# Kernel optimization log

Hardware: AMD Instinct MI355X
Metric: run time of the kernel (lower is better)

Reference implementation:

```python
import jax, jax.numpy as jnp
import numpy as np


def _bilinear_grid_sample(fea, grid):
    """torch.nn.functional.grid_sample, mode=bilinear, padding_mode=zeros, align_corners=False.
    fea: (B,C,H,W); grid: (B,Hg,Wg,2) with xy in [-1,1]. Returns (B,C,Hg,Wg)."""
    B, C, H, W = fea.shape
    Hg, Wg = grid.shape[1], grid.shape[2]
    gx, gy = grid[..., 0], grid[..., 1]
    # unnormalize (align_corners=False)
    x = ((gx + 1.0) * W - 1.0) * 0.5
    y = ((gy + 1.0) * H - 1.0) * 0.5
    x0 = jnp.floor(x); y0 = jnp.floor(y)
    x1 = x0 + 1.0;     y1 = y0 + 1.0
    wx1 = x - x0; wx0 = 1.0 - wx1
    wy1 = y - y0; wy0 = 1.0 - wy1
    flat = fea.reshape(B, C, H * W)

    def corner(xi, yi, w):
        valid = (xi >= 0) & (xi <= W - 1) & (yi >= 0) & (yi <= H - 1)
        xi_c = jnp.clip(xi, 0, W - 1).astype(jnp.int32)
        yi_c = jnp.clip(yi, 0, H - 1).astype(jnp.int32)
        idx = (yi_c * W + xi_c).reshape(B, 1, Hg * Wg)
        v = jnp.take_along_axis(flat, jnp.broadcast_to(idx, (B, C, Hg * Wg)), axis=2)
        return v * (w * valid.astype(fea.dtype)).reshape(B, 1, Hg * Wg)

    out = (corner(x0, y0, wx0 * wy0) + corner(x1, y0, wx1 * wy0)
           + corner(x0, y1, wx0 * wy1) + corner(x1, y1, wx1 * wy1))
    return out.reshape(B, C, Hg, Wg)


def _conv1d_k1(x, W, b):
    # x: (B,Cin,N), W: (Cout,Cin), b: (Cout,) -> (B,Cout,N)
    return jnp.einsum('oc,bcn->bon', W, x) + b[None, :, None]


def setup_inputs() -> dict:
    key = jax.random.key(0)
    ks = jax.random.split(key, 8)
    B, C, H, W = 4, 16, 90, 160
    N_s, N_anchor, N_y = 8, 200, 20
    scale = 8
    fea = jax.random.normal(ks[0], (B, C, H, W), dtype=jnp.float32)
    sampled_3d_points = jax.random.normal(ks[1], (N_s, B, N_anchor, N_y, 4), dtype=jnp.float32)
    # 2D pixel coords at full resolution: x in [0, W*scale), y in [0, H*scale)
    u = jax.random.uniform(ks[2], (N_s, B, N_anchor, N_y, 2), dtype=jnp.float32)
    points_2d_coord = u * jnp.array([W * scale, H * scale], dtype=jnp.float32)
    W_local = jax.random.normal(ks[3], (16, 16), dtype=jnp.float32) * 0.25
    b_local = jax.random.normal(ks[4], (16,), dtype=jnp.float32) * 0.01
    W_emb = jax.random.normal(ks[5], (256, 4), dtype=jnp.float32) * 0.5
    b_emb = jax.random.normal(ks[6], (256,), dtype=jnp.float32) * 0.01
    return {"fea": fea, "sampled_3d_points": sampled_3d_points,
            "points_2d_coord": points_2d_coord,
            "W_local": W_local, "b_local": b_local,
            "W_emb": W_emb, "b_emb": b_emb, "scale": scale}


def reference(fea, sampled_3d_points, points_2d_coord, W_local, b_local, W_emb, b_emb, scale):
    B, C, H, W = fea.shape
    N_s, _, N_anchor, N_y, _ = points_2d_coord.shape
    # normalize 2D coords to [-1,1] grid
    norm_weight = jnp.array([1.0 / W, 1.0 / H], dtype=fea.dtype)
    ner = (points_2d_coord / scale) * norm_weight * 2.0 - 1.0
    ner = jnp.transpose(ner, (1, 0, 2, 3, 4)).reshape(B, N_s * N_anchor, N_y, 2)
    local_fea = _bilinear_grid_sample(fea, ner)            # (B,C,N_s*N_anchor,N_y)
    local_fea = local_fea.reshape(B, C, -1)                # (B,C,N)
    local_fea = _conv1d_k1(local_fea, W_local, b_local)    # (B,16,N)
    # point embedding: permute(1,4,0,2,3) -> (B,4,N_s,N_anchor,N_y)
    sp = jnp.transpose(sampled_3d_points, (1, 4, 0, 2, 3)).reshape(B, 4, -1)
    embedded_points = _conv1d_k1(sp, W_emb, b_emb)         # (B,256,N)
    return (embedded_points, local_fea)
```

## Files before the change

### kernel.cpp

```cpp
#include <hip/hip_runtime.h>

#define B_    4
#define C_    16
#define H_    90
#define W_    160
#define NS_   8
#define NA_   200
#define NY_   20
#define NPB_  (NS_*NA_*NY_)
#define NPB4_ (NPB_/4)
#define CO_   256
#define EMB_ELEMS ((size_t)B_*CO_*NPB_)
#define SCALE_F 8.0f
#define HW_   (H_*W_)

#define EMB_BLOCKS 1000
#define LOC_BLOCKS 500
#define TOTAL_BLOCKS (EMB_BLOCKS + LOC_BLOCKS)

typedef float f32x4 __attribute__((ext_vector_type(4)));

__device__ __forceinline__ void nt_store4(const float4& v, float4* dst) {
    f32x4 r = { v.x, v.y, v.z, v.w };
    __builtin_nontemporal_store(r, (f32x4*)dst);
}

__global__ __launch_bounds__(256) void fused_local_emb_kernel(
    const float*  __restrict__ fea,
    const float4* __restrict__ sp3d,
    const float2* __restrict__ pc2d,
    const float*  __restrict__ W_local,
    const float*  __restrict__ b_local,
    const float4* __restrict__ W_emb,
    const float*  __restrict__ b_emb,
    float* __restrict__ out)
{
    __shared__ float  sPx[256], sPy[256], sPz[256], sPw[256];
    __shared__ float4 sWe[128];
    __shared__ float  sbe[128];
    __shared__ float sWl[256];
    __shared__ float sbl[16];
    __shared__ float sV[16*256];

    const int tid = threadIdx.x;
    const int idx = blockIdx.x;
    const int l  = tid & 63;
    const int wv = tid >> 6;

    const int grp = idx / 3;
    const int r3  = idx - grp*3;

    if (r3 != 2) {
        const int emb_id = grp*2 + r3;
        const int b    = emb_id / 250;
        const int rem0 = emb_id - b*250;
        const int tile = rem0 >> 1;
        const int half = rem0 & 1;

        if (tid < 128) {
            sWe[tid] = W_emb[half*128 + tid];
            sbe[tid] = b_emb[half*128 + tid];
        }

        const int n = tile*256 + tid;
        const int s = n / (NA_*NY_);
        const int r = n - s*(NA_*NY_);
        const float4 p = sp3d[s*(B_*NA_*NY_) + b*(NA_*NY_) + r];
        sPx[tid] = p.x; sPy[tid] = p.y; sPz[tid] = p.z; sPw[tid] = p.w;
        __syncthreads();

        const float4 PX = ((const float4*)sPx)[l];
        const float4 PY = ((const float4*)sPy)[l];
        const float4 PZ = ((const float4*)sPz)[l];
        const float4 PW = ((const float4*)sPw)[l];

        float4* eo4 = (float4*)(out + (size_t)b*CO_*NPB_) + tile*64;
        const int m0 = wv*32;
#pragma unroll 8
        for (int oi = 0; oi < 32; ++oi) {
            const int m = m0 + oi;
            const int o = half*128 + m;
            const float4 w = sWe[m];
            const float bb = sbe[m];
            float4 rr;
            rr.x = fmaf(w.w, PW.x, fmaf(w.z, PZ.x, fmaf(w.y, PY.x, fmaf(w.x, PX.x, bb))));
            rr.y = fmaf(w.w, PW.y, fmaf(w.z, PZ.y, fmaf(w.y, PY.y, fmaf(w.x, PX.y, bb))));
            rr.z = fmaf(w.w, PW.z, fmaf(w.z, PZ.z, fmaf(w.y, PY.z, fmaf(w.x, PX.z, bb))));
            rr.w = fmaf(w.w, PW.w, fmaf(w.z, PZ.w, fmaf(w.y, PY.w, fmaf(w.x, PX.w, bb))));
            nt_store4(rr, &eo4[(size_t)o*NPB4_ + l]);
        }
        return;
    }

    const int lid  = grp;
    const int b    = lid / 125;
    const int tile = lid - b*125;
    const int n    = tile*256 + tid;

    sWl[tid] = W_local[tid];
    if (tid < 16) sbl[tid] = b_local[tid];

    const int s   = n / (NA_*NY_);
    const int rem = n - s*(NA_*NY_);
    const int a   = rem / NY_;
    const int yy  = rem - a*NY_;

    const float2 pc = pc2d[((s*B_ + b)*NA_ + a)*NY_ + yy];

    const float gx = (pc.x / SCALE_F) * (1.0f/(float)W_) * 2.0f - 1.0f;
    const float gy = (pc.y / SCALE_F) * (1.0f/(float)H_) * 2.0f - 1.0f;
    const float xf = ((gx + 1.0f) * (float)W_ - 1.0f) * 0.5f;
    const float yf = ((gy + 1.0f) * (float)H_ - 1.0f) * 0.5f;

    const float x0f = floorf(xf), y0f = floorf(yf);
    const float x1f = x0f + 1.0f, y1f = y0f + 1.0f;
    const float wx1 = xf - x0f, wx0 = 1.0f - wx1;
    const float wy1 = yf - y0f, wy0 = 1.0f - wy1;

    const float vx0 = (x0f >= 0.0f && x0f <= (float)(W_-1)) ? 1.0f : 0.0f;
    const float vx1 = (x1f >= 0.0f && x1f <= (float)(W_-1)) ? 1.0f : 0.0f;
    const float vy0 = (y0f >= 0.0f && y0f <= (float)(H_-1)) ? 1.0f : 0.0f;
    const float vy1 = (y1f >= 0.0f && y1f <= (float)(H_-1)) ? 1.0f : 0.0f;

    const int xi0 = (int)fminf(fmaxf(x0f, 0.0f), (float)(W_-1));
    const int xi1 = (int)fminf(fmaxf(x1f, 0.0f), (float)(W_-1));
    const int yi0 = (int)fminf(fmaxf(y0f, 0.0f), (float)(H_-1));
    const int yi1 = (int)fminf(fmaxf(y1f, 0.0f), (float)(H_-1));

    const float w00 = wx0*wy0*vx0*vy0;
    const float w01 = wx1*wy0*vx1*vy0;
    const float w10 = wx0*wy1*vx0*vy1;
    const float w11 = wx1*wy1*vx1*vy1;

    const int i00 = yi0*W_ + xi0;
    const int i01 = yi0*W_ + xi1;
    const int i10 = yi1*W_ + xi0;
    const int i11 = yi1*W_ + xi1;

    const float* fb = fea + b*(C_*HW_);
    float f00[16], f01[16], f10[16], f11[16];
#pragma unroll
    for (int c = 0; c < 16; ++c) {
        const float* fc = fb + c*HW_;
        f00[c] = fc[i00];
        f01[c] = fc[i01];
        f10[c] = fc[i10];
        f11[c] = fc[i11];
    }

    float v[16];
#pragma unroll
    for (int c = 0; c < 16; ++c)
        v[c] = w00*f00[c] + w01*f01[c] + w10*f10[c] + w11*f11[c];
#pragma unroll
    for (int c = 0; c < 16; ++c)
        sV[c*256 + tid] = v[c];

    __syncthreads();

    float4 acc[4];
#pragma unroll
    for (int k = 0; k < 4; ++k) {
        const float bk = sbl[4*wv + k];
        acc[k].x = bk; acc[k].y = bk; acc[k].z = bk; acc[k].w = bk;
    }
#pragma unroll
    for (int c = 0; c < 16; ++c) {
        const float4 sv = ((const float4*)(sV + c*256))[l];
#pragma unroll
        for (int k = 0; k < 4; ++k) {
            const float wl = sWl[(4*wv + k)*16 + c];
            acc[k].x = fmaf(wl, sv.x, acc[k].x);
            acc[k].y = fmaf(wl, sv.y, acc[k].y);
            acc[k].z = fmaf(wl, sv.z, acc[k].z);
            acc[k].w = fmaf(wl, sv.w, acc[k].w);
        }
    }
    float4* lo4 = (float4*)(out + EMB_ELEMS + (size_t)b*16*NPB_ + tile*256);
#pragma unroll
    for (int k = 0; k < 4; ++k)
        nt_store4(acc[k], &lo4[(4*wv + k)*NPB4_ + l]);
}

extern "C" void kernel_launch(void* const* d_in, const int* in_sizes, int n_in,
                              void* d_out, int out_size, void* d_ws, size_t ws_size,
                              hipStream_t stream) {
    const float* fea     = (const float*)d_in[0];
    const float4* sp3d   = (const float4*)d_in[1];
    const float2* pc2d   = (const float2*)d_in[2];
    const float* W_local = (const float*)d_in[3];
    const float* b_local = (const float*)d_in[4];
    const float4* W_emb  = (const float4*)d_in[5];
    const float* b_emb   = (const float*)d_in[6];

    dim3 grid(TOTAL_BLOCKS);
    dim3 block(256);
    fused_local_emb_kernel<<<grid, block, 0, stream>>>(
        fea, sp3d, pc2d, W_local, b_local, W_emb, b_emb, (float*)d_out);
}
```

Baseline: 36.98 us.

## Merge grid-sample work into half of the embedding blocks to overlap gathers with stores

```diff
diff --git a/kernel.cpp b/kernel.cpp
--- a/kernel.cpp
+++ b/kernel.cpp
@@ -14,9 +14,7 @@
 #define SCALE_F 8.0f
 #define HW_   (H_*W_)
 
-#define EMB_BLOCKS 1000
-#define LOC_BLOCKS 500
-#define TOTAL_BLOCKS (EMB_BLOCKS + LOC_BLOCKS)
+#define TOTAL_BLOCKS 1000
 
 typedef float f32x4 __attribute__((ext_vector_type(4)));
 
@@ -38,148 +36,140 @@
     __shared__ float  sPx[256], sPy[256], sPz[256], sPw[256];
     __shared__ float4 sWe[128];
     __shared__ float  sbe[128];
-    __shared__ float sWl[256];
-    __shared__ float sbl[16];
-    __shared__ float sV[16*256];
+    __shared__ float  sWl[256];
+    __shared__ float  sbl[16];
+    __shared__ float  sV[16*256];
 
     const int tid = threadIdx.x;
-    const int idx = blockIdx.x;
+    const int blk = blockIdx.x;
+    const int b    = blk / 250;
+    const int rem0 = blk - b*250;
+    const int tile = rem0 >> 1;
+    const int half = rem0 & 1;
     const int l  = tid & 63;
     const int wv = tid >> 6;
 
-    const int grp = idx / 3;
-    const int r3  = idx - grp*3;
-
-    if (r3 != 2) {
-        const int emb_id = grp*2 + r3;
-        const int b    = emb_id / 250;
-        const int rem0 = emb_id - b*250;
-        const int tile = rem0 >> 1;
-        const int half = rem0 & 1;
-
-        if (tid < 128) {
-            sWe[tid] = W_emb[half*128 + tid];
-            sbe[tid] = b_emb[half*128 + tid];
-        }
-
-        const int n = tile*256 + tid;
-        const int s = n / (NA_*NY_);
-        const int r = n - s*(NA_*NY_);
-        const float4 p = sp3d[s*(B_*NA_*NY_) + b*(NA_*NY_) + r];
-        sPx[tid] = p.x; sPy[tid] = p.y; sPz[tid] = p.z; sPw[tid] = p.w;
-        __syncthreads();
-
-        const float4 PX = ((const float4*)sPx)[l];
-        const float4 PY = ((const float4*)sPy)[l];
-        const float4 PZ = ((const float4*)sPz)[l];
-        const float4 PW = ((const float4*)sPw)[l];
-
-        float4* eo4 = (float4*)(out + (size_t)b*CO_*NPB_) + tile*64;
-        const int m0 = wv*32;
-#pragma unroll 8
-        for (int oi = 0; oi < 32; ++oi) {
-            const int m = m0 + oi;
-            const int o = half*128 + m;
-            const float4 w = sWe[m];
-            const float bb = sbe[m];
-            float4 rr;
-            rr.x = fmaf(w.w, PW.x, fmaf(w.z, PZ.x, fmaf(w.y, PY.x, fmaf(w.x, PX.x, bb))));
-            rr.y = fmaf(w.w, PW.y, fmaf(w.z, PZ.y, fmaf(w.y, PY.y, fmaf(w.x, PX.y, bb))));
-            rr.z = fmaf(w.w, PW.z, fmaf(w.z, PZ.z, fmaf(w.y, PY.z, fmaf(w.x, PX.z, bb))));
-            rr.w = fmaf(w.w, PW.w, fmaf(w.z, PZ.w, fmaf(w.y, PY.w, fmaf(w.x, PX.w, bb))));
-            nt_store4(rr, &eo4[(size_t)o*NPB4_ + l]);
-        }
-        return;
+    if (tid < 128) {
+        sWe[tid] = W_emb[half*128 + tid];
+        sbe[tid] = b_emb[half*128 + tid];
+    }
+    if (half == 0) {
+        sWl[tid] = W_local[tid];
+        if (tid < 16) sbl[tid] = b_local[tid];
     }
 
-    const int lid  = grp;
-    const int b    = lid / 125;
-    const int tile = lid - b*125;
-    const int n    = tile*256 + tid;
+    const int n = tile*256 + tid;
+    const int s = n / (NA_*NY_);
+    const int r = n - s*(NA_*NY_);
+    const int pidx = s*(B_*NA_*NY_) + b*(NA_*NY_) + r;
+    const float4 p = sp3d[pidx];
+    sPx[tid] = p.x; sPy[tid] = p.y; sPz[tid] = p.z; sPw[tid] = p.w;
 
-    sWl[tid] = W_local[tid];
-    if (tid < 16) sbl[tid] = b_local[tid];
+    float w00=0.f, w01=0.f, w10=0.f, w11=0.f;
+    int i00=0, i01=0, i10=0, i11=0;
+    if (half == 0) {
+        const float2 pc = pc2d[pidx];
+        const float gx = (pc.x / SCALE_F) * (1.0f/(float)W_) * 2.0f - 1.0f;
+        const float gy = (pc.y / SCALE_F) * (1.0f/(float)H_) * 2.0f - 1.0f;
+        const float xf = ((gx + 1.0f) * (float)W_ - 1.0f) * 0.5f;
+        const float yf = ((gy + 1.0f) * (float)H_ - 1.0f) * 0.5f;
 
-    const int s   = n / (NA_*NY_);
-    const int rem = n - s*(NA_*NY_);
-    const int a   = rem / NY_;
-    const int yy  = rem - a*NY_;
+        const float x0f = floorf(xf), y0f = floorf(yf);
+        const float x1f = x0f + 1.0f, y1f = y0f + 1.0f;
+        const float wx1 = xf - x0f, wx0 = 1.0f - wx1;
+        const float wy1 = yf - y0f, wy0 = 1.0f - wy1;
 
-    const float2 pc = pc2d[((s*B_ + b)*NA_ + a)*NY_ + yy];
+        const float vx0 = (x0f >= 0.0f && x0f <= (float)(W_-1)) ? 1.0f : 0.0f;
+        const float vx1 = (x1f >= 0.0f && x1f <= (float)(W_-1)) ? 1.0f : 0.0f;
+        const float vy0 = (y0f >= 0.0f && y0f <= (float)(H_-1)) ? 1.0f : 0.0f;
+        const float vy1 = (y1f >= 0.0f && y1f <= (float)(H_-1)) ? 1.0f : 0.0f;
 
-    const float gx = (pc.x / SCALE_F) * (1.0f/(float)W_) * 2.0f - 1.0f;
-    const float gy = (pc.y / SCALE_F) * (1.0f/(float)H_) * 2.0f - 1.0f;
-    const float xf = ((gx + 1.0f) * (float)W_ - 1.0f) * 0.5f;
-    const float yf = ((gy + 1.0f) * (float)H_ - 1.0f) * 0.5f;
+        const int xi0 = (int)fminf(fmaxf(x0f, 0.0f), (float)(W_-1));
+        const int xi1 = (int)fminf(fmaxf(x1f, 0.0f), (float)(W_-1));
+        const int yi0 = (int)fminf(fmaxf(y0f, 0.0f), (float)(H_-1));
+        const int yi1 = (int)fminf(fmaxf(y1f, 0.0f), (float)(H_-1));
 
-    const float x0f = floorf(xf), y0f = floorf(yf);
-    const float x1f = x0f + 1.0f, y1f = y0f + 1.0f;
-    const float wx1 = xf - x0f, wx0 = 1.0f - wx1;
-    const float wy1 = yf - y0f, wy0 = 1.0f - wy1;
+        w00 = wx0*wy0*vx0*vy0;
+        w01 = wx1*wy0*vx1*vy0;
+        w10 = wx0*wy1*vx0*vy1;
+        w11 = wx1*wy1*vx1*vy1;
 
-    const float vx0 = (x0f >= 0.0f && x0f <= (float)(W_-1)) ? 1.0f : 0.0f;
-    const float vx1 = (x1f >= 0.0f && x1f <= (float)(W_-1)) ? 1.0f : 0.0f;
-    const float vy0 = (y0f >= 0.0f && y0f <= (float)(H_-1)) ? 1.0f : 0.0f;
-    const float vy1 = (y1f >= 0.0f && y1f <= (float)(H_-1)) ? 1.0f : 0.0f;
-
-    const int xi0 = (int)fminf(fmaxf(x0f, 0.0f), (float)(W_-1));
-    const int xi1 = (int)fminf(fmaxf(x1f, 0.0f), (float)(W_-1));
-    const int yi0 = (int)fminf(fmaxf(y0f, 0.0f), (float)(H_-1));
-    const int yi1 = (int)fminf(fmaxf(y1f, 0.0f), (float)(H_-1));
-
-    const float w00 = wx0*wy0*vx0*vy0;
-    const float w01 = wx1*wy0*vx1*vy0;
-    const float w10 = wx0*wy1*vx0*vy1;
-    const float w11 = wx1*wy1*vx1*vy1;
-
-    const int i00 = yi0*W_ + xi0;
-    const int i01 = yi0*W_ + xi1;
-    const int i10 = yi1*W_ + xi0;
-    const int i11 = yi1*W_ + xi1;
-
-    const float* fb = fea + b*(C_*HW_);
-    float f00[16], f01[16], f10[16], f11[16];
-#pragma unroll
-    for (int c = 0; c < 16; ++c) {
-        const float* fc = fb + c*HW_;
-        f00[c] = fc[i00];
-        f01[c] = fc[i01];
-        f10[c] = fc[i10];
-        f11[c] = fc[i11];
+        i00 = yi0*W_ + xi0;
+        i01 = yi0*W_ + xi1;
+        i10 = yi1*W_ + xi0;
+        i11 = yi1*W_ + xi1;
     }
-
-    float v[16];
-#pragma unroll
-    for (int c = 0; c < 16; ++c)
-        v[c] = w00*f00[c] + w01*f01[c] + w10*f10[c] + w11*f11[c];
-#pragma unroll
-    for (int c = 0; c < 16; ++c)
-        sV[c*256 + tid] = v[c];
 
     __syncthreads();
 
-    float4 acc[4];
+    float f00[16], f01[16], f10[16], f11[16];
+    if (half == 0) {
+        const float* fb = fea + b*(C_*HW_);
 #pragma unroll
-    for (int k = 0; k < 4; ++k) {
-        const float bk = sbl[4*wv + k];
-        acc[k].x = bk; acc[k].y = bk; acc[k].z = bk; acc[k].w = bk;
+        for (int c = 0; c < 16; ++c) {
+            const float* fc = fb + c*HW_;
+            f00[c] = fc[i00];
+            f01[c] = fc[i01];
+            f10[c] = fc[i10];
+            f11[c] = fc[i11];
+        }
     }
+
+    const float4 PX = ((const float4*)sPx)[l];
+    const float4 PY = ((const float4*)sPy)[l];
+    const float4 PZ = ((const float4*)sPz)[l];
+    const float4 PW = ((const float4*)sPw)[l];
+
+    float4* eo4 = (float4*)(out + (size_t)b*CO_*NPB_) + tile*64;
+    const int m0 = wv*32;
+#pragma unroll 8
+    for (int oi = 0; oi < 32; ++oi) {
+        const int m = m0 + oi;
+        const int o = half*128 + m;
+        const float4 w = sWe[m];
+        const float bb = sbe[m];
+        float4 rr;
+        rr.x = fmaf(w.w, PW.x, fmaf(w.z, PZ.x, fmaf(w.y, PY.x, fmaf(w.x, PX.x, bb))));
+        rr.y = fmaf(w.w, PW.y, fmaf(w.z, PZ.y, fmaf(w.y, PY.y, fmaf(w.x, PX.y, bb))));
+        rr.z = fmaf(w.w, PW.z, fmaf(w.z, PZ.z, fmaf(w.y, PY.z, fmaf(w.x, PX.z, bb))));
+        rr.w = fmaf(w.w, PW.w, fmaf(w.z, PZ.w, fmaf(w.y, PY.w, fmaf(w.x, PX.w, bb))));
+        nt_store4(rr, &eo4[(size_t)o*NPB4_ + l]);
+    }
+
+    if (half == 0) {
+        float v[16];
 #pragma unroll
-    for (int c = 0; c < 16; ++c) {
-        const float4 sv = ((const float4*)(sV + c*256))[l];
+        for (int c = 0; c < 16; ++c)
+            v[c] = w00*f00[c] + w01*f01[c] + w10*f10[c] + w11*f11[c];
+#pragma unroll
+        for (int c = 0; c < 16; ++c)
+            sV[c*256 + tid] = v[c];
+
+        __syncthreads();
+
+        float4 acc[4];
 #pragma unroll
         for (int k = 0; k < 4; ++k) {
-            const float wl = sWl[(4*wv + k)*16 + c];
-            acc[k].x = fmaf(wl, sv.x, acc[k].x);
-            acc[k].y = fmaf(wl, sv.y, acc[k].y);
-            acc[k].z = fmaf(wl, sv.z, acc[k].z);
-            acc[k].w = fmaf(wl, sv.w, acc[k].w);
+            const float bk = sbl[4*wv + k];
+            acc[k].x = bk; acc[k].y = bk; acc[k].z = bk; acc[k].w = bk;
         }
+#pragma unroll
+        for (int c = 0; c < 16; ++c) {
+            const float4 sv = ((const float4*)(sV + c*256))[l];
+#pragma unroll
+            for (int k = 0; k < 4; ++k) {
+                const float wl = sWl[(4*wv + k)*16 + c];
+                acc[k].x = fmaf(wl, sv.x, acc[k].x);
+                acc[k].y = fmaf(wl, sv.y, acc[k].y);
+                acc[k].z = fmaf(wl, sv.z, acc[k].z);
+                acc[k].w = fmaf(wl, sv.w, acc[k].w);
+            }
+        }
+        float4* lo4 = (float4*)(out + EMB_ELEMS + (size_t)b*16*NPB_ + tile*256);
+#pragma unroll
+        for (int k = 0; k < 4; ++k)
+            nt_store4(acc[k], &lo4[(4*wv + k)*NPB4_ + l]);
     }
-    float4* lo4 = (float4*)(out + EMB_ELEMS + (size_t)b*16*NPB_ + tile*256);
-#pragma unroll
-    for (int k = 0; k < 4; ++k)
-        nt_store4(acc[k], &lo4[(4*wv + k)*NPB4_ + l]);
 }
 
 extern "C" void kernel_launch(void* const* d_in, const int* in_sizes, int n_in,
```

Result: slower. 51.10 us (+38.2%).
